# Kernel optimization log

Measured on AMD Instinct MI355X. Metric: run time of the kernel, lower is better.

The kernel has to match this reference:

```python
import jax, jax.numpy as jnp
import numpy as np

NUM_HEADS = 16
EMBED = 1024


def setup_inputs() -> dict:
    key = jax.random.key(0)
    k1, k2, k3 = jax.random.split(key, 3)
    B, T, L = 2, 2048, EMBED
    x = jax.random.normal(k1, (B, T, L), dtype=jnp.float32)
    # Dense kernels (use_bias=False), scaled like lecun init
    W_attn = jax.random.normal(k2, (L, 3 * L), dtype=jnp.float32) / np.sqrt(L)
    W_proj = jax.random.normal(k3, (L, L), dtype=jnp.float32) / np.sqrt(L)
    return {"x": x, "W_attn": W_attn, "W_proj": W_proj}


def reference(x, W_attn, W_proj):
    B, T, L = x.shape
    H = NUM_HEADS
    Dh = L // H
    qkv = x @ W_attn                       # [B, T, 3L]
    q, k, v = jnp.split(qkv, 3, axis=2)
    # [B, T, L] -> [B, H, T, Dh]
    q = q.reshape(B, T, H, Dh).transpose(0, 2, 1, 3)
    k = k.reshape(B, T, H, Dh).transpose(0, 2, 1, 3)
    v = v.reshape(B, T, H, Dh).transpose(0, 2, 1, 3)
    # NOTE: faithful to the source, scale is rsqrt(full embedding size L), not head dim
    att = jnp.einsum('bhqd,bhkd->bhqk', q, k) * jax.lax.rsqrt(jnp.float32(L))
    causal = jnp.tril(jnp.ones((T, T), dtype=bool))[None, None]
    att = jnp.where(causal, att, float('-inf'))
    att = jax.nn.softmax(att, axis=-1)
    y = jnp.einsum('bhqk,bhkd->bhqd', att, v)      # [B, H, T, Dh]
    y = y.transpose(0, 2, 1, 3).reshape(B, T, L)
    return y @ W_proj
```

## Files before the change

### kernel.cpp

```cpp
#include <hip/hip_runtime.h>
#include <math.h>

typedef unsigned short u16;
typedef unsigned int u32;
typedef short short8 __attribute__((ext_vector_type(8)));
typedef float f32x4 __attribute__((ext_vector_type(4)));
typedef float f4 __attribute__((ext_vector_type(4)));
typedef unsigned short u16x4 __attribute__((ext_vector_type(4)));
typedef unsigned int u32x2 __attribute__((ext_vector_type(2)));

__device__ __forceinline__ u16 f2bf(float f) {
  unsigned u = __builtin_bit_cast(unsigned, f);
  u += 0x7fffu + ((u >> 16) & 1u);
  return (u16)(u >> 16);
}

__device__ __forceinline__ float bf2f(u16 v) {
  return __builtin_bit_cast(float, (u32)v << 16);
}

__device__ __forceinline__ u32 cvtpk_bf16(float a, float b) {
  u32 r;
  asm("v_cvt_pk_bf16_f32 %0, %1, %2" : "=v"(r) : "v"(a), "v"(b));
  return r;
}

__device__ __forceinline__ float exp2r(float x) {
  float r;
  asm("v_exp_f32 %0, %1" : "=v"(r) : "v"(x));
  return r;
}

__device__ __forceinline__ void gload16(const void* g, void* l) {
  __builtin_amdgcn_global_load_lds((const __attribute__((address_space(1))) void*)g,
                                   (__attribute__((address_space(3))) void*)l, 16, 0, 0);
}

__global__ __launch_bounds__(256) void prep_kernel(const float* __restrict__ x,
                                                   u16* __restrict__ xb,
                                                   const float* __restrict__ Wa,
                                                   u16* __restrict__ Wat,
                                                   const float* __restrict__ Wp,
                                                   u16* __restrict__ Wpt, float qscale) {
  __shared__ float t[32][33];
  const int bx = blockIdx.x, tid = threadIdx.x;
  if (bx < 1024) {
    const int n4 = 4194304 / 4;
    for (int i = bx * 256 + tid; i < n4; i += 1024 * 256) {
      f4 v = ((const f4*)x)[i];
      u16x4 o;
      o[0] = f2bf(v[0]); o[1] = f2bf(v[1]); o[2] = f2bf(v[2]); o[3] = f2bf(v[3]);
      ((u16x4*)xb)[i] = o;
    }
    return;
  }
  const float* in;
  u16* out;
  int R, C, j0, i0, qcols;
  if (bx < 4096) {
    int bid = bx - 1024;
    in = Wa; out = Wat; R = 1024; C = 3072; qcols = 1024;
    j0 = (bid % 96) * 32; i0 = (bid / 96) * 32;
  } else {
    int bid = bx - 4096;
    in = Wp; out = Wpt; R = 1024; C = 1024; qcols = 0;
    j0 = (bid % 32) * 32; i0 = (bid / 32) * 32;
  }
  const int tx = tid & 31, ty = tid >> 5;
#pragma unroll
  for (int k = 0; k < 4; ++k) t[ty + 8 * k][tx] = in[(size_t)(i0 + ty + 8 * k) * C + j0 + tx];
  __syncthreads();
#pragma unroll
  for (int k = 0; k < 4; ++k) {
    int orow = j0 + ty + 8 * k;
    float v = t[tx][ty + 8 * k];
    if (orow < qcols) v *= qscale;
    out[(size_t)orow * R + i0 + tx] = f2bf(v);
  }
}

template <int MODE>
__global__ __launch_bounds__(256) void gemm_kernel(const u16* __restrict__ A,
                                                   const u16* __restrict__ Bt,
                                                   void* __restrict__ Cv,
                                                   u16* __restrict__ Vt, int N, int K) {
  __shared__ __align__(16) u16 lA[128 * 64];
  __shared__ __align__(16) u16 lB[128 * 64];
  const int tid = threadIdx.x;
  const int w = tid >> 6, lane = tid & 63, lo = lane & 15, hi = lane >> 4;
  const int wm = w >> 1, wn = w & 1;
  const int m0 = blockIdx.y * 128, n0 = blockIdx.x * 128;
  f32x4 acc[4][4] = {};
  const int nkt = K >> 6;
  for (int kt = 0; kt < nkt; ++kt) {
    const int k0 = kt * 64;
#pragma unroll
    for (int c = 0; c < 4; ++c) {
      int flat = tid + c * 256;
      int r = flat >> 3, kc = flat & 7;
      int kcs = kc ^ (r & 7);
      gload16(A + (size_t)(m0 + r) * K + k0 + kcs * 8, (char*)lA + flat * 16);
      gload16(Bt + (size_t)(n0 + r) * K + k0 + kcs * 8, (char*)lB + flat * 16);
    }
    __syncthreads();
#pragma unroll
    for (int kk = 0; kk < 2; ++kk) {
      short8 af[4], bf[4];
#pragma unroll
      for (int mf = 0; mf < 4; ++mf) {
        int row = wm * 64 + mf * 16 + lo;
        int addr = (row * 128 + kk * 64 + hi * 16) ^ ((row & 7) << 4);
        af[mf] = *(const short8*)((const char*)lA + addr);
      }
#pragma unroll
      for (int nf = 0; nf < 4; ++nf) {
        int row = wn * 64 + nf * 16 + lo;
        int addr = (row * 128 + kk * 64 + hi * 16) ^ ((row & 7) << 4);
        bf[nf] = *(const short8*)((const char*)lB + addr);
      }
#pragma unroll
      for (int mf = 0; mf < 4; ++mf)
#pragma unroll
        for (int nf = 0; nf < 4; ++nf)
          acc[mf][nf] = __builtin_amdgcn_mfma_f32_16x16x32_bf16(af[mf], bf[nf], acc[mf][nf], 0, 0, 0);
    }
    __syncthreads();
  }
#pragma unroll
  for (int mf = 0; mf < 4; ++mf)
#pragma unroll
    for (int nf = 0; nf < 4; ++nf) {
      const int row0 = m0 + wm * 64 + mf * 16 + hi * 4;
      const int col = n0 + wn * 64 + nf * 16 + lo;
      if (MODE == 0) {
#pragma unroll
        for (int r = 0; r < 4; ++r)
          ((float*)Cv)[(size_t)(row0 + r) * N + col] = acc[mf][nf][r];
      } else {
        if (col < 2048) {
#pragma unroll
          for (int r = 0; r < 4; ++r)
            ((u16*)Cv)[(size_t)(row0 + r) * N + col] = f2bf(acc[mf][nf][r]);
        } else {
          const int dl = col - 2048;
          const int bh = (row0 >> 11) * 16 + (dl >> 6);
          const int d = dl & 63, t = row0 & 2047;
          u16x4 pk;
#pragma unroll
          for (int r = 0; r < 4; ++r) pk[r] = f2bf(acc[mf][nf][r]);
          *(u16x4*)&Vt[(size_t)bh * 131072 + d * 2048 + t] = pk;
        }
      }
    }
}

__global__ __launch_bounds__(256) void gemm_proj(const u16* __restrict__ A,
                                                 const u16* __restrict__ Bt,
                                                 float* __restrict__ C, int N, int K) {
  __shared__ __align__(16) u16 lA[128 * 64];
  __shared__ __align__(16) u16 lB[64 * 64];
  const int tid = threadIdx.x;
  const int w = tid >> 6, lane = tid & 63, lo = lane & 15, hi = lane >> 4;
  const int wm = w >> 1, wn = w & 1;
  const int m0 = blockIdx.y * 128, n0 = blockIdx.x * 64;
  f32x4 acc[4][2] = {};
  const int nkt = K >> 6;
  for (int kt = 0; kt < nkt; ++kt) {
    const int k0 = kt * 64;
#pragma unroll
    for (int c = 0; c < 4; ++c) {
      int flat = tid + c * 256;
      int r = flat >> 3, kc = flat & 7;
      int kcs = kc ^ (r & 7);
      gload16(A + (size_t)(m0 + r) * K + k0 + kcs * 8, (char*)lA + flat * 16);
    }
#pragma unroll
    for (int c = 0; c < 2; ++c) {
      int flat = tid + c * 256;
      int r = flat >> 3, kc = flat & 7;
      int kcs = kc ^ (r & 7);
      gload16(Bt + (size_t)(n0 + r) * K + k0 + kcs * 8, (char*)lB + flat * 16);
    }
    __syncthreads();
#pragma unroll
    for (int kk = 0; kk < 2; ++kk) {
      short8 af[4], bf[2];
#pragma unroll
      for (int mf = 0; mf < 4; ++mf) {
        int row = wm * 64 + mf * 16 + lo;
        int addr = (row * 128 + kk * 64 + hi * 16) ^ ((row & 7) << 4);
        af[mf] = *(const short8*)((const char*)lA + addr);
      }
#pragma unroll
      for (int nf = 0; nf < 2; ++nf) {
        int row = wn * 32 + nf * 16 + lo;
        int addr = (row * 128 + kk * 64 + hi * 16) ^ ((row & 7) << 4);
        bf[nf] = *(const short8*)((const char*)lB + addr);
      }
#pragma unroll
      for (int mf = 0; mf < 4; ++mf)
#pragma unroll
        for (int nf = 0; nf < 2; ++nf)
          acc[mf][nf] = __builtin_amdgcn_mfma_f32_16x16x32_bf16(af[mf], bf[nf], acc[mf][nf], 0, 0, 0);
    }
    __syncthreads();
  }
#pragma unroll
  for (int mf = 0; mf < 4; ++mf)
#pragma unroll
    for (int nf = 0; nf < 2; ++nf) {
      const int row0 = m0 + wm * 64 + mf * 16 + hi * 4;
      const int col = n0 + wn * 32 + nf * 16 + lo;
#pragma unroll
      for (int r = 0; r < 4; ++r)
        C[(size_t)(row0 + r) * N + col] = acc[mf][nf][r];
    }
}

__global__ __launch_bounds__(256) void attn_kernel(const u16* __restrict__ qkv,
                                                   const u16* __restrict__ Vt,
                                                   u16* __restrict__ yb) {
  __shared__ __align__(16) u16 lK[2][64 * 64];
  __shared__ __align__(16) u16 lV[2][64 * 64];
  __shared__ __align__(16) u16 pl[4][32][72];
  const int tid = threadIdx.x, w = tid >> 6, lane = tid & 63;
  const int lo = lane & 15, hi = lane >> 4;
  const int id = blockIdx.x;
  const int j = id >> 5;
  const int qb = (j < 8) ? (15 - 2 * j) : (2 * (j - 8));
  const int bh = id & 31, b = bh >> 4, h = bh & 15;
  const int wq0 = qb * 128 + w * 32;

  int kSrc[2], vSrc[2];
#pragma unroll
  for (int c = 0; c < 2; ++c) {
    const int flat = tid + c * 256;
    const int sr = flat >> 3, skc = flat & 7;
    const int skcs = (skc ^ (sr & 7)) * 8;
    kSrc[c] = (b * 2048 + sr) * 3072 + 1024 + h * 64 + skcs;
    vSrc[c] = bh * 131072 + sr * 2048 + skcs;
  }

  short8 qf[2][2];
#pragma unroll
  for (int m = 0; m < 2; ++m) {
    const int qbase = (b * 2048 + wq0 + m * 16 + lo) * 3072 + h * 64 + hi * 8;
    qf[m][0] = *(const short8*)(qkv + qbase);
    qf[m][1] = *(const short8*)(qkv + qbase + 32);
  }

  short8 vones;
#pragma unroll
  for (int i = 0; i < 8; ++i) vones[i] = (short)0x3F80;

  f32x4 yacc[2][4] = {};
  f32x4 lacc[2] = {};

  const int nt = 2 * qb + 2;
#pragma unroll
  for (int c = 0; c < 2; ++c) {
    gload16(qkv + kSrc[c], (char*)lK[0] + (tid + c * 256) * 16);
    gload16(Vt + vSrc[c], (char*)lV[0] + (tid + c * 256) * 16);
  }
  asm volatile("s_waitcnt vmcnt(0)" ::: "memory");
  __syncthreads();

  int buf = 0;
#pragma unroll 1
  for (int it = 0; it < nt; ++it) {
    const int t0 = it * 64;
    if (it + 1 < nt) {
#pragma unroll
      for (int c = 0; c < 2; ++c) {
        gload16(qkv + (kSrc[c] + (t0 + 64) * 3072), (char*)lK[buf ^ 1] + (tid + c * 256) * 16);
        gload16(Vt + (vSrc[c] + t0 + 64), (char*)lV[buf ^ 1] + (tid + c * 256) * 16);
      }
    }
    if (t0 <= wq0 + 31) {
      const char* lKb = (const char*)lK[buf];
      const char* lVb = (const char*)lV[buf];
      f32x4 st[4][2] = {};
#pragma unroll
      for (int kk = 0; kk < 2; ++kk) {
        short8 kf[4];
#pragma unroll
        for (int n = 0; n < 4; ++n)
          kf[n] = *(const short8*)(lKb + ((n * 16 + lo) * 128 + (((kk * 4 + hi) ^ (lo & 7)) * 16)));
#pragma unroll
        for (int n = 0; n < 4; ++n)
#pragma unroll
          for (int m = 0; m < 2; ++m)
            st[n][m] = __builtin_amdgcn_mfma_f32_16x16x32_bf16(kf[n], qf[m][kk], st[n][m], 0, 0, 0);
      }

      if (t0 + 63 > wq0) {
#pragma unroll
        for (int m = 0; m < 2; ++m) {
          const int q = wq0 + m * 16 + lo;
#pragma unroll
          for (int n = 0; n < 4; ++n)
#pragma unroll
            for (int r = 0; r < 4; ++r) {
              const int k = t0 + n * 16 + hi * 4 + r;
              st[n][m][r] = (k <= q) ? st[n][m][r] : -INFINITY;
            }
        }
      }
#pragma unroll
      for (int m = 0; m < 2; ++m)
#pragma unroll
        for (int n = 0; n < 4; ++n) {
          u32x2 pw;
          pw[0] = cvtpk_bf16(exp2r(st[n][m][0]), exp2r(st[n][m][1]));
          pw[1] = cvtpk_bf16(exp2r(st[n][m][2]), exp2r(st[n][m][3]));
          *(u32x2*)&pl[w][m * 16 + lo][n * 16 + hi * 4] = pw;
        }
      short8 pa0[2], pa1[2];
#pragma unroll
      for (int m = 0; m < 2; ++m) {
        pa0[m] = *(const short8*)&pl[w][m * 16 + lo][hi * 8];
        pa1[m] = *(const short8*)&pl[w][m * 16 + lo][32 + hi * 8];
      }
      short8 vf0[4], vf1[4];
#pragma unroll
      for (int nf = 0; nf < 4; ++nf) {
        vf0[nf] = *(const short8*)(lVb + ((nf * 16 + lo) * 128 + (((hi) ^ (lo & 7)) * 16)));
        vf1[nf] = *(const short8*)(lVb + ((nf * 16 + lo) * 128 + (((4 + hi) ^ (lo & 7)) * 16)));
      }
#pragma unroll
      for (int m = 0; m < 2; ++m) {
#pragma unroll
        for (int nf = 0; nf < 4; ++nf)
          yacc[m][nf] = __builtin_amdgcn_mfma_f32_16x16x32_bf16(pa0[m], vf0[nf], yacc[m][nf], 0, 0, 0);
        lacc[m] = __builtin_amdgcn_mfma_f32_16x16x32_bf16(pa0[m], vones, lacc[m], 0, 0, 0);
      }
#pragma unroll
      for (int m = 0; m < 2; ++m) {
#pragma unroll
        for (int nf = 0; nf < 4; ++nf)
          yacc[m][nf] = __builtin_amdgcn_mfma_f32_16x16x32_bf16(pa1[m], vf1[nf], yacc[m][nf], 0, 0, 0);
        lacc[m] = __builtin_amdgcn_mfma_f32_16x16x32_bf16(pa1[m], vones, lacc[m], 0, 0, 0);
      }
    }
    asm volatile("s_waitcnt vmcnt(0)" ::: "memory");
    __syncthreads();
    buf ^= 1;
  }

#pragma unroll
  for (int m = 0; m < 2; ++m) {
    f32x4 inv;
#pragma unroll
    for (int r = 0; r < 4; ++r) inv[r] = 1.f / lacc[m][r];
#pragma unroll
    for (int nf = 0; nf < 4; ++nf)
#pragma unroll
      for (int r = 0; r < 4; ++r)
        yb[(b * 2048 + wq0 + m * 16 + hi * 4 + r) * 1024 + h * 64 + nf * 16 + lo] =
            f2bf(yacc[m][nf][r] * inv[r]);
  }
}

extern "C" void kernel_launch(void* const* d_in, const int* in_sizes, int n_in,
                              void* d_out, int out_size, void* d_ws, size_t ws_size,
                              hipStream_t stream) {
  const float* x = (const float*)d_in[0];
  const float* Wa = (const float*)d_in[1];
  const float* Wp = (const float*)d_in[2];
  char* ws = (char*)d_ws;
  u16* xb   = (u16*)(ws);
  u16* Wat  = (u16*)(ws + 8388608);
  u16* Wpt  = (u16*)(ws + 14680064);
  u16* qkvb = (u16*)(ws + 16777216);
  u16* Vt   = (u16*)(ws + 41943040);
  u16* yb   = (u16*)(ws + 50331648);

  const float CS = 0.03125f * 1.44269504088896f;
  prep_kernel<<<5120, 256, 0, stream>>>(x, xb, Wa, Wat, Wp, Wpt, CS);
  gemm_kernel<2><<<dim3(24, 32), 256, 0, stream>>>(xb, Wat, (void*)qkvb, Vt, 3072, 1024);
  attn_kernel<<<512, 256, 0, stream>>>(qkvb, Vt, yb);
  gemm_proj<<<dim3(16, 32), 256, 0, stream>>>(yb, Wpt, (float*)d_out, 1024, 1024);
}
```

Measured before the change: 107.3 us.

## Keep softmax probabilities in registers via permuted V layout; XCD-aware QKV GEMM tiling

The QKV GEMM now writes V-transposed with a permuted token order so that the exp'd score fragments produced by the QK^T MFMA can be packed directly into the A-operand layout of the PV MFMA. This removes the per-wave LDS round trip for P (stores, reads and the pl buffer). The QKV GEMM also switches to a 1D grid with a block-index remap that groups tiles per XCD for L2 locality. The risk is that the token permutation must exactly match the MFMA fragment layout, otherwise the output is silently wrong.

```diff
diff --git a/kernel.cpp b/kernel.cpp
--- a/kernel.cpp
+++ b/kernel.cpp
@@ -7,16 +7,12 @@
 typedef float f32x4 __attribute__((ext_vector_type(4)));
 typedef float f4 __attribute__((ext_vector_type(4)));
 typedef unsigned short u16x4 __attribute__((ext_vector_type(4)));
-typedef unsigned int u32x2 __attribute__((ext_vector_type(2)));
+typedef unsigned int u32x4 __attribute__((ext_vector_type(4)));
 
 __device__ __forceinline__ u16 f2bf(float f) {
   unsigned u = __builtin_bit_cast(unsigned, f);
   u += 0x7fffu + ((u >> 16) & 1u);
   return (u16)(u >> 16);
-}
-
-__device__ __forceinline__ float bf2f(u16 v) {
-  return __builtin_bit_cast(float, (u32)v << 16);
 }
 
 __device__ __forceinline__ u32 cvtpk_bf16(float a, float b) {
@@ -79,17 +75,20 @@
   }
 }
 
-template <int MODE>
-__global__ __launch_bounds__(256) void gemm_kernel(const u16* __restrict__ A,
-                                                   const u16* __restrict__ Bt,
-                                                   void* __restrict__ Cv,
-                                                   u16* __restrict__ Vt, int N, int K) {
+__global__ __launch_bounds__(256) void gemm_qkv(const u16* __restrict__ A,
+                                                const u16* __restrict__ Bt,
+                                                u16* __restrict__ qkvb,
+                                                u16* __restrict__ Vt, int N, int K) {
   __shared__ __align__(16) u16 lA[128 * 64];
   __shared__ __align__(16) u16 lB[128 * 64];
   const int tid = threadIdx.x;
   const int w = tid >> 6, lane = tid & 63, lo = lane & 15, hi = lane >> 4;
   const int wm = w >> 1, wn = w & 1;
-  const int m0 = blockIdx.y * 128, n0 = blockIdx.x * 128;
+  const int id = blockIdx.x;
+  const int xcd = id & 7, kk0 = id >> 3;
+  const int py = kk0 & 7, px = kk0 >> 3;
+  const int m0 = (8 * (xcd >> 1) + py) * 128;
+  const int n0 = (12 * (xcd & 1) + px) * 128;
   f32x4 acc[4][4] = {};
   const int nkt = K >> 6;
   for (int kt = 0; kt < nkt; ++kt) {
@@ -132,24 +131,20 @@
     for (int nf = 0; nf < 4; ++nf) {
       const int row0 = m0 + wm * 64 + mf * 16 + hi * 4;
       const int col = n0 + wn * 64 + nf * 16 + lo;
-      if (MODE == 0) {
+      if (col < 2048) {
 #pragma unroll
         for (int r = 0; r < 4; ++r)
-          ((float*)Cv)[(size_t)(row0 + r) * N + col] = acc[mf][nf][r];
+          qkvb[(size_t)(row0 + r) * N + col] = f2bf(acc[mf][nf][r]);
       } else {
-        if (col < 2048) {
-#pragma unroll
-          for (int r = 0; r < 4; ++r)
-            ((u16*)Cv)[(size_t)(row0 + r) * N + col] = f2bf(acc[mf][nf][r]);
-        } else {
-          const int dl = col - 2048;
-          const int bh = (row0 >> 11) * 16 + (dl >> 6);
-          const int d = dl & 63, t = row0 & 2047;
-          u16x4 pk;
-#pragma unroll
-          for (int r = 0; r < 4; ++r) pk[r] = f2bf(acc[mf][nf][r]);
-          *(u16x4*)&Vt[(size_t)bh * 131072 + d * 2048 + t] = pk;
-        }
+        const int dl = col - 2048;
+        const int bh = (row0 >> 11) * 16 + (dl >> 6);
+        const int d = dl & 63, t4 = row0 & 2047;
+        const int p4 = (t4 & ~63) + 32 * ((t4 >> 5) & 1) + 8 * ((t4 >> 2) & 3) +
+                       4 * ((t4 >> 4) & 1);
+        u16x4 pk;
+#pragma unroll
+        for (int r = 0; r < 4; ++r) pk[r] = f2bf(acc[mf][nf][r]);
+        *(u16x4*)&Vt[(size_t)bh * 131072 + d * 2048 + p4] = pk;
       }
     }
 }
@@ -222,7 +217,6 @@
                                                    u16* __restrict__ yb) {
   __shared__ __align__(16) u16 lK[2][64 * 64];
   __shared__ __align__(16) u16 lV[2][64 * 64];
-  __shared__ __align__(16) u16 pl[4][32][72];
   const int tid = threadIdx.x, w = tid >> 6, lane = tid & 63;
   const int lo = lane & 15, hi = lane >> 4;
   const int id = blockIdx.x;
@@ -279,13 +273,14 @@
     if (t0 <= wq0 + 31) {
       const char* lKb = (const char*)lK[buf];
       const char* lVb = (const char*)lV[buf];
+      const int sw = lo & 7;
       f32x4 st[4][2] = {};
 #pragma unroll
       for (int kk = 0; kk < 2; ++kk) {
         short8 kf[4];
 #pragma unroll
         for (int n = 0; n < 4; ++n)
-          kf[n] = *(const short8*)(lKb + ((n * 16 + lo) * 128 + (((kk * 4 + hi) ^ (lo & 7)) * 16)));
+          kf[n] = *(const short8*)(lKb + ((n * 16 + lo) * 128 + (((kk * 4 + hi) ^ sw) * 16)));
 #pragma unroll
         for (int n = 0; n < 4; ++n)
 #pragma unroll
@@ -306,40 +301,38 @@
             }
         }
       }
-#pragma unroll
-      for (int m = 0; m < 2; ++m)
-#pragma unroll
-        for (int n = 0; n < 4; ++n) {
-          u32x2 pw;
-          pw[0] = cvtpk_bf16(exp2r(st[n][m][0]), exp2r(st[n][m][1]));
-          pw[1] = cvtpk_bf16(exp2r(st[n][m][2]), exp2r(st[n][m][3]));
-          *(u32x2*)&pl[w][m * 16 + lo][n * 16 + hi * 4] = pw;
+
+      short8 pa[2][2];
+#pragma unroll
+      for (int m = 0; m < 2; ++m) {
+        u32x4 w0, w1;
+#pragma unroll
+        for (int n = 0; n < 2; ++n) {
+          w0[2 * n]     = cvtpk_bf16(exp2r(st[n][m][0]), exp2r(st[n][m][1]));
+          w0[2 * n + 1] = cvtpk_bf16(exp2r(st[n][m][2]), exp2r(st[n][m][3]));
         }
-      short8 pa0[2], pa1[2];
-#pragma unroll
-      for (int m = 0; m < 2; ++m) {
-        pa0[m] = *(const short8*)&pl[w][m * 16 + lo][hi * 8];
-        pa1[m] = *(const short8*)&pl[w][m * 16 + lo][32 + hi * 8];
-      }
-      short8 vf0[4], vf1[4];
-#pragma unroll
-      for (int nf = 0; nf < 4; ++nf) {
-        vf0[nf] = *(const short8*)(lVb + ((nf * 16 + lo) * 128 + (((hi) ^ (lo & 7)) * 16)));
-        vf1[nf] = *(const short8*)(lVb + ((nf * 16 + lo) * 128 + (((4 + hi) ^ (lo & 7)) * 16)));
-      }
-#pragma unroll
-      for (int m = 0; m < 2; ++m) {
+#pragma unroll
+        for (int n = 0; n < 2; ++n) {
+          w1[2 * n]     = cvtpk_bf16(exp2r(st[n + 2][m][0]), exp2r(st[n + 2][m][1]));
+          w1[2 * n + 1] = cvtpk_bf16(exp2r(st[n + 2][m][2]), exp2r(st[n + 2][m][3]));
+        }
+        pa[m][0] = __builtin_bit_cast(short8, w0);
+        pa[m][1] = __builtin_bit_cast(short8, w1);
+      }
+
+#pragma unroll
+      for (int hh = 0; hh < 2; ++hh) {
+        short8 vf[4];
 #pragma unroll
         for (int nf = 0; nf < 4; ++nf)
-          yacc[m][nf] = __builtin_amdgcn_mfma_f32_16x16x32_bf16(pa0[m], vf0[nf], yacc[m][nf], 0, 0, 0);
-        lacc[m] = __builtin_amdgcn_mfma_f32_16x16x32_bf16(pa0[m], vones, lacc[m], 0, 0, 0);
-      }
-#pragma unroll
-      for (int m = 0; m < 2; ++m) {
-#pragma unroll
-        for (int nf = 0; nf < 4; ++nf)
-          yacc[m][nf] = __builtin_amdgcn_mfma_f32_16x16x32_bf16(pa1[m], vf1[nf], yacc[m][nf], 0, 0, 0);
-        lacc[m] = __builtin_amdgcn_mfma_f32_16x16x32_bf16(pa1[m], vones, lacc[m], 0, 0, 0);
+          vf[nf] = *(const short8*)(lVb + ((nf * 16 + lo) * 128 + (((hh * 4 + hi) ^ sw) * 16)));
+#pragma unroll
+        for (int m = 0; m < 2; ++m) {
+#pragma unroll
+          for (int nf = 0; nf < 4; ++nf)
+            yacc[m][nf] = __builtin_amdgcn_mfma_f32_16x16x32_bf16(pa[m][hh], vf[nf], yacc[m][nf], 0, 0, 0);
+          lacc[m] = __builtin_amdgcn_mfma_f32_16x16x32_bf16(pa[m][hh], vones, lacc[m], 0, 0, 0);
+        }
       }
     }
     asm volatile("s_waitcnt vmcnt(0)" ::: "memory");
@@ -377,7 +370,7 @@
 
   const float CS = 0.03125f * 1.44269504088896f;
   prep_kernel<<<5120, 256, 0, stream>>>(x, xb, Wa, Wat, Wp, Wpt, CS);
-  gemm_kernel<2><<<dim3(24, 32), 256, 0, stream>>>(xb, Wat, (void*)qkvb, Vt, 3072, 1024);
+  gemm_qkv<<<768, 256, 0, stream>>>(xb, Wat, qkvb, Vt, 3072, 1024);
   attn_kernel<<<512, 256, 0, stream>>>(qkvb, Vt, yb);
   gemm_proj<<<dim3(16, 32), 256, 0, stream>>>(yb, Wpt, (float*)d_out, 1024, 1024);
 }
```

Measured after the change: 103.0 us. 1.04x faster.
